# Optimization experiments

Hardware: AMD Instinct MI355X
Metric: run time of the kernel (lower is better)

The kernel has to match this reference:

```python
import jax, jax.numpy as jnp
import numpy as np

FRACTAL_OUTPUT = (5, 5)            # (a, b); requires 5 * num_kernels == a*b
PERC_THRESHOLD = 0.59275
NEXT_SHAPE = (224, 224)
K_END = int(0.4 * FRACTAL_OUTPUT[0] * FRACTAL_OUTPUT[1] + 1)   # 11
KERNEL_SIZES = list(range(3, K_END + 1, 2))                    # [3,5,7,9,11]


def setup_inputs() -> dict:
    key = jax.random.key(0)
    inputs = jax.random.uniform(key, (64, 224, 224, 3), dtype=jnp.float32) * 255.0
    return {"inputs": inputs}


def _extract_patches(x, k):
    # tf.image.extract_patches(sizes=strides=k, SAME) == zero-pad + space-to-depth
    B, H, W, C = x.shape
    rows, cols = -(-H // k), -(-W // k)
    ph, pw = rows * k - H, cols * k - W
    x = jnp.pad(x, ((0, 0), (ph // 2, ph - ph // 2), (pw // 2, pw - pw // 2), (0, 0)))
    x = x.reshape(B, rows, k, cols, k, C).transpose(0, 1, 3, 2, 4, 5)
    return x.reshape(B * rows * cols, k, k, C), rows * cols


def _binarize(patches, k, ch):
    # distance function: 1 iff |channel value - center pixel channel value| <= k
    center = patches[:, k // 2, k // 2, ch][:, None, None]
    return (jnp.abs(patches[..., ch] - center) <= k).astype(jnp.int32)


def _connected_stats(binp, k):
    # 4-connected components via min-label propagation (== tfa connected_components
    # up to relabeling; we only need #components and max label count incl. background)
    N = binp.shape[0]
    idx = jnp.arange(1, k * k + 1, dtype=jnp.int32).reshape(k, k)
    INF = jnp.int32(k * k + 2)
    lbl0 = jnp.where(binp > 0, idx, 0)

    def step(_, lbl):
        v = jnp.where(binp > 0, lbl, INF)
        pad = lambda a, w: jnp.pad(a, ((0, 0),) + w, constant_values=INF)
        up    = pad(v, ((1, 0), (0, 0)))[:, :-1, :]
        down  = pad(v, ((0, 1), (0, 0)))[:, 1:, :]
        left  = pad(v, ((0, 0), (1, 0)))[:, :, :-1]
        right = pad(v, ((0, 0), (0, 1)))[:, :, 1:]
        m = jnp.minimum(jnp.minimum(v, up), jnp.minimum(jnp.minimum(down, left), right))
        return jnp.where(binp > 0, m, 0)

    lbl = jax.lax.fori_loop(0, k * k, step, lbl0)  # k*k iters guarantee convergence
    ncomp = jnp.sum((binp > 0) & (lbl == idx), axis=(1, 2)).astype(jnp.int32)
    lblf = lbl.reshape(N, k * k)
    cnt = jnp.zeros((N, k * k + 1), jnp.int32).at[jnp.arange(N)[:, None], lblf].add(1)
    return ncomp, cnt.max(axis=1)  # (#components, most-common label count incl bg 0)


def _components(inputs, k, ch):
    B = inputs.shape[0]
    patches, P = _extract_patches(inputs, k)
    binp = _binarize(patches, k, ch)                    # (B*P, k, k)
    ones = binp.sum(axis=(1, 2)).reshape(B, P)          # int counts per patch
    # tf.bincount(minlength=1, maxlength=k*k): bins 0..k*k-1, value k*k dropped
    cnt = jnp.zeros((B, k * k + 1), jnp.float32).at[jnp.arange(B)[:, None], ones].add(1.0)
    prob = cnt[:, : k * k] / P                          # (B, k*k)
    n = jnp.arange(1, k * k + 1, dtype=jnp.float32)
    fd = (prob / n).sum(1)
    m = (prob * n).sum(1)
    m2 = ((prob * prob) * n).sum(1)
    lac = (m2 - m * m) / (m * m)
    perc = ((ones.astype(jnp.float32) / (k * k)) >= PERC_THRESHOLD).astype(jnp.int32)
    acp = perc.sum(1) // P                              # tf integer reduce_mean
    ncomp, marea = _connected_stats(binp, k)
    acn = ncomp.reshape(B, P).sum(1) // P
    acma = marea.reshape(B, P).sum(1) // P
    return jnp.stack([acn.astype(jnp.float32), acp.astype(jnp.float32),
                      acma.astype(jnp.float32), lac, fd], axis=1)   # (B, 5)


def _rearrange(c):
    # group metric-major: all acn over kernels, then acp, acma, lac, fd
    return jnp.concatenate([c[:, mm::5] for mm in range(5)], axis=1)


def reference(inputs):
    B = inputs.shape[0]
    chans = []
    for ch in range(3):
        comps = jnp.concatenate([_components(inputs, k, ch) for k in KERNEL_SIZES], axis=1)
        chans.append(_rearrange(comps).reshape(B, FRACTAL_OUTPUT[0], FRACTAL_OUTPUT[1]))
    out = jnp.stack(chans, axis=3)                      # (B, a, b, 3)
    return jax.image.resize(out, (B, NEXT_SHAPE[0], NEXT_SHAPE[1], 3), method='bilinear')
```

## Files before the change

kernel.cpp:

```cpp
#include <hip/hip_runtime.h>

#define HW 224
#define NIMG 64
#define NPIX ((size_t)NIMG * HW * HW)

typedef unsigned long long u64;

struct U128 { u64 lo, hi; };

__device__ __forceinline__ u64  u_or  (u64 a, u64 b){ return a | b; }
__device__ __forceinline__ u64  u_and (u64 a, u64 b){ return a & b; }
__device__ __forceinline__ u64  u_andn(u64 a, u64 b){ return a & ~b; }
__device__ __forceinline__ bool u_eq(u64 a, u64 b){ return a == b; }
__device__ __forceinline__ bool u_nz(u64 a){ return a != 0ull; }
__device__ __forceinline__ u64  u_shl(u64 a, int n){ return a << n; }
__device__ __forceinline__ u64  u_shr(u64 a, int n){ return a >> n; }
__device__ __forceinline__ int  u_pop(u64 a){ return __popcll(a); }
__device__ __forceinline__ u64  u_low(u64 a){ return a & (0ull - a); }

__device__ __forceinline__ U128 u_or  (U128 a, U128 b){ return {a.lo|b.lo, a.hi|b.hi}; }
__device__ __forceinline__ U128 u_and (U128 a, U128 b){ return {a.lo&b.lo, a.hi&b.hi}; }
__device__ __forceinline__ U128 u_andn(U128 a, U128 b){ return {a.lo&~b.lo, a.hi&~b.hi}; }
__device__ __forceinline__ bool u_eq(U128 a, U128 b){ return a.lo==b.lo && a.hi==b.hi; }
__device__ __forceinline__ bool u_nz(U128 a){ return (a.lo | a.hi) != 0ull; }
__device__ __forceinline__ U128 u_shl(U128 a, int n){
    return { a.lo << n, (a.hi << n) | (a.lo >> (64 - n)) };
}
__device__ __forceinline__ U128 u_shr(U128 a, int n){
    return { (a.lo >> n) | (a.hi << (64 - n)), a.hi >> n };
}
__device__ __forceinline__ int u_pop(U128 a){ return __popcll(a.lo) + __popcll(a.hi); }
__device__ __forceinline__ U128 u_low(U128 a){
    if (a.lo) return { a.lo & (0ull - a.lo), 0ull };
    return { 0ull, a.hi & (0ull - a.hi) };
}

template<bool B, class T, class F> struct sel        { using type = T; };
template<class T, class F>         struct sel<false, T, F> { using type = F; };

template<int K>
__device__ __forceinline__ void load_row(const float* __restrict__ p, float* r) {
#pragma unroll
    for (int j = 0; j + 4 <= K; j += 4) {
        float4 v; __builtin_memcpy(&v, p + j, 16);
        r[j] = v.x; r[j + 1] = v.y; r[j + 2] = v.z; r[j + 3] = v.w;
    }
    if constexpr ((K & 3) >= 2) {
        constexpr int b = (K / 4) * 4;
        float2 v; __builtin_memcpy(&v, p + b, 8);
        r[b] = v.x; r[b + 1] = v.y;
    }
    if constexpr (K & 1) r[K - 1] = p[K - 1];
}

template<int K, int S>
__device__ __forceinline__ void stats_body(const float* __restrict__ img,
                                           float* __restrict__ o,
                                           int hist[4][124], int* sums) {
    constexpr int KK   = K * K;
    constexpr int ROWS = (HW + K - 1) / K;
    constexpr int P    = ROWS * ROWS;
    constexpr int PAD  = (ROWS * K - HW) / 2;
    using M = typename sel<(KK <= 64), u64, U128>::type;
    const int wid = threadIdx.x >> 6;

    u64 lcl = 0, lch = 0, rcl = 0, rch = 0;
#pragma unroll
    for (int i = 0; i < K; i++) {
        const int cl = i * K, cr = i * K + K - 1;
        if (cl < 64) lcl |= 1ull << cl; else lch |= 1ull << (cl - 64);
        if (cr < 64) rcl |= 1ull << cr; else rch |= 1ull << (cr - 64);
    }
    M leftCol, rightCol;
    if constexpr (KK <= 64) { leftCol = lcl; rightCol = rcl; }
    else { leftCol = U128{lcl, lch}; rightCol = U128{rcl, rch}; }

    int t_perc = 0, t_ncomp = 0, t_marea = 0;

    for (int p = threadIdx.x; p < P; p += 256) {
        const int pr = p / ROWS, pc = p - pr * ROWS;
        const int y0 = pr * K - PAD, x0 = pc * K - PAD;
        const float cen = img[((size_t)(y0 + K / 2) * HW + (x0 + K / 2)) * S];

        M msk;
        if constexpr (KK <= 64) msk = 0ull; else msk = U128{0, 0};

        const bool fast = (S == 1) && (y0 >= 0) && (x0 >= 0) &&
                          (y0 + K <= HW) && (x0 + K <= HW);
        if (fast) {
#pragma unroll
            for (int i = 0; i < K; i++) {
                float r[K];
                load_row<K>(img + (size_t)(y0 + i) * HW + x0, r);
#pragma unroll
                for (int j = 0; j < K; j++) {
                    const u64 bit = (fabsf(r[j] - cen) <= (float)K) ? 1ull : 0ull;
                    const int cb = i * K + j;
                    if constexpr (KK <= 64) msk |= bit << cb;
                    else { if (cb < 64) msk.lo |= bit << cb; else msk.hi |= bit << (cb - 64); }
                }
            }
        } else {
#pragma unroll
            for (int i = 0; i < K; i++) {
                const int y = y0 + i;
                const bool yin = (unsigned)y < (unsigned)HW;
#pragma unroll
                for (int j = 0; j < K; j++) {
                    const int x = x0 + j;
                    const bool inb = yin && ((unsigned)x < (unsigned)HW);
                    const float v = inb ? img[((size_t)y * HW + x) * S] : 0.0f;
                    const u64 bit = (fabsf(v - cen) <= (float)K) ? 1ull : 0ull;
                    const int cb = i * K + j;
                    if constexpr (KK <= 64) msk |= bit << cb;
                    else { if (cb < 64) msk.lo |= bit << cb; else msk.hi |= bit << (cb - 64); }
                }
            }
        }
        const int ones = u_pop(msk);

        M nbm = u_or(u_or(u_shl(u_andn(msk, rightCol), 1),
                          u_shr(u_andn(msk, leftCol ), 1)),
                     u_or(u_shl(msk, K), u_shr(msk, K)));
        M iso = u_andn(msk, nbm);
        const int niso = u_pop(iso);
        int ncomp = niso, maxsz = (niso > 0) ? 1 : 0;
        M m = u_andn(msk, iso);
        while (u_nz(m)) {
            M s = u_low(m);
            for (;;) {
                M g = u_or(s, u_or(u_or(u_shl(u_andn(s, rightCol), 1),
                                        u_shr(u_andn(s, leftCol ), 1)),
                                   u_or(u_shl(s, K), u_shr(s, K))));
                g = u_and(g, m);
                if (u_eq(g, s)) break;
                s = g;
            }
            ncomp++;
            const int sz = u_pop(s);
            if (sz > maxsz) maxsz = sz;
            m = u_andn(m, s);
        }

        const int bgcnt = KK - ones;
        const int marea = (bgcnt > maxsz) ? bgcnt : maxsz;

        t_ncomp += ncomp;
        t_marea += marea;
        if ((float)ones / (float)KK >= 0.59275f) t_perc++;
        atomicAdd(&hist[wid][ones], 1);
    }

    atomicAdd(&sums[0], t_perc);
    atomicAdd(&sums[1], t_ncomp);
    atomicAdd(&sums[2], t_marea);
    __syncthreads();

    if (threadIdx.x == 0) {
        const float Pf = (float)P;
        float fd = 0.0f, m1 = 0.0f, m2 = 0.0f;
        for (int s = 0; s < KK; s++) {
            const float prob = (float)(hist[0][s] + hist[1][s] + hist[2][s] + hist[3][s]) / Pf;
            const float n = (float)(s + 1);
            fd += prob / n;
            m1 += prob * n;
            m2 += prob * prob * n;
        }
        const float lac = (m2 - m1 * m1) / (m1 * m1);
        o[0]  = (float)(sums[1] / P);
        o[15] = (float)(sums[0] / P);
        o[30] = (float)(sums[2] / P);
        o[45] = lac;
        o[60] = fd;
    }
}

template<int S>
__global__ __launch_bounds__(256) void fractal_stats(const float* __restrict__ in,
                                                     float* __restrict__ interm) {
    const int b    = blockIdx.x / 15;
    const int rem  = blockIdx.x % 15;
    const int ch   = rem / 5;
    const int kidx = rem % 5;

    __shared__ int hist[4][124];
    __shared__ int sums[3];
    for (int i = threadIdx.x; i < 4 * 124; i += 256) ((int*)hist)[i] = 0;
    if (threadIdx.x < 3) sums[threadIdx.x] = 0;
    __syncthreads();

    const float* img = (S == 1) ? in + ((size_t)ch * NIMG + b) * HW * HW
                                : in + (size_t)b * HW * HW * 3 + ch;
    float* o = interm + (size_t)b * 75 + kidx * 3 + ch;

    switch (kidx) {
        case 0: stats_body<3,  S>(img, o, hist, sums); break;
        case 1: stats_body<5,  S>(img, o, hist, sums); break;
        case 2: stats_body<7,  S>(img, o, hist, sums); break;
        case 3: stats_body<9,  S>(img, o, hist, sums); break;
        case 4: stats_body<11, S>(img, o, hist, sums); break;
    }
}

__global__ __launch_bounds__(256) void deinterleave(const float* __restrict__ in,
                                                    float* __restrict__ planes) {
    const size_t pix = ((size_t)blockIdx.x * 256 + threadIdx.x) * 4;
    if (pix >= NPIX) return;
    float4 a, b, c;
    __builtin_memcpy(&a, in + pix * 3,     16);
    __builtin_memcpy(&b, in + pix * 3 + 4, 16);
    __builtin_memcpy(&c, in + pix * 3 + 8, 16);
    const float4 p0 = make_float4(a.x, a.w, b.z, c.y);
    const float4 p1 = make_float4(a.y, b.x, b.w, c.z);
    const float4 p2 = make_float4(a.z, b.y, c.x, c.w);
    __builtin_memcpy(planes + pix,            &p0, 16);
    __builtin_memcpy(planes + NPIX + pix,     &p1, 16);
    __builtin_memcpy(planes + 2 * NPIX + pix, &p2, 16);
}

__global__ __launch_bounds__(256) void fractal_resize(const float* __restrict__ interm,
                                                      float* __restrict__ out, int total) {
    const int idx = blockIdx.x * 256 + threadIdx.x;
    if (idx >= total) return;
    const int ch = idx % 3;
    int t = idx / 3;
    const int x = t % HW; t /= HW;
    const int y = t % HW;
    const int b = t / HW;

    const float sc = 5.0f / 224.0f;
    const float uy = ((float)y + 0.5f) * sc - 0.5f;
    const float ux = ((float)x + 0.5f) * sc - 0.5f;

    const float fy = floorf(uy), fx = floorf(ux);
    const float wy = uy - fy,    wx = ux - fx;
    int y0 = (int)fy, x0 = (int)fx;
    int y1 = y0 + 1,  x1 = x0 + 1;
    if (y0 < 0) y0 = 0; if (x0 < 0) x0 = 0;
    if (y1 > 4) y1 = 4; if (x1 > 4) x1 = 4;

    const float* g = interm + (size_t)b * 75 + ch;
    const float v00 = g[(y0 * 5 + x0) * 3];
    const float v01 = g[(y0 * 5 + x1) * 3];
    const float v10 = g[(y1 * 5 + x0) * 3];
    const float v11 = g[(y1 * 5 + x1) * 3];

    out[idx] = (1.0f - wy) * ((1.0f - wx) * v00 + wx * v01)
             +         wy  * ((1.0f - wx) * v10 + wx * v11);
}

extern "C" void kernel_launch(void* const* d_in, const int* in_sizes, int n_in,
                              void* d_out, int out_size, void* d_ws, size_t ws_size,
                              hipStream_t stream) {
    const float* in = (const float*)d_in[0];
    float* out = (float*)d_out;
    float* interm = (float*)d_ws;

    const size_t planes_off = 19456;
    const size_t need = planes_off + 3 * NPIX * sizeof(float);

    if (ws_size >= need) {
        float* planes = (float*)((char*)d_ws + planes_off);
        deinterleave<<<(int)(NPIX / 4 / 256), 256, 0, stream>>>(in, planes);
        fractal_stats<1><<<NIMG * 15, 256, 0, stream>>>(planes, interm);
    } else {
        fractal_stats<3><<<NIMG * 15, 256, 0, stream>>>(in, interm);
    }
    fractal_resize<<<(out_size + 255) / 256, 256, 0, stream>>>(interm, out, out_size);
}
```

Baseline: 177.6 us.

## Split patch work into 8 slices per combo with 64-thread blocks and global accumulation

The stats kernel now launches 7680 single-wavefront blocks instead of 960 256-thread blocks. Each block handles one eighth of the patches of one (image, channel, kernel) combination and merges its histogram and sums into a global int accumulator with atomics. A new finalize kernel then computes the lacunarity, fractal dimension and averages from that accumulator. The aim is better load balance and occupancy across CUs, because small-K combos previously had uneven per-block work. In exchange it adds one extra kernel launch, global atomics, and accumulator zeroing folded into the deinterleave kernel.

```diff
diff --git a/kernel.cpp b/kernel.cpp
--- a/kernel.cpp
+++ b/kernel.cpp
@@ -3,6 +3,10 @@
 #define HW 224
 #define NIMG 64
 #define NPIX ((size_t)NIMG * HW * HW)
+#define NSLICE 8
+#define ACC_STRIDE 128
+#define NCOMBO (NIMG * 15)
+#define ACC_BYTES (NCOMBO * ACC_STRIDE * 4)
 
 typedef unsigned long long u64;
 
@@ -53,103 +57,223 @@
     if constexpr (K & 1) r[K - 1] = p[K - 1];
 }
 
-template<int K, int S>
-__device__ __forceinline__ void stats_body(const float* __restrict__ img,
-                                           float* __restrict__ o,
-                                           int hist[4][124], int* sums) {
+template<int K, int S, class M>
+__device__ __forceinline__ void do_patch(const float* __restrict__ img, int p,
+                                         M leftCol, M rightCol,
+                                         int* hist, int& t_perc, int& t_ncomp,
+                                         int& t_marea) {
     constexpr int KK   = K * K;
     constexpr int ROWS = (HW + K - 1) / K;
-    constexpr int P    = ROWS * ROWS;
     constexpr int PAD  = (ROWS * K - HW) / 2;
-    using M = typename sel<(KK <= 64), u64, U128>::type;
-    const int wid = threadIdx.x >> 6;
-
-    u64 lcl = 0, lch = 0, rcl = 0, rch = 0;
+
+    const int pr = p / ROWS, pc = p - pr * ROWS;
+    const int y0 = pr * K - PAD, x0 = pc * K - PAD;
+    const float cen = img[((size_t)(y0 + K / 2) * HW + (x0 + K / 2)) * S];
+
+    M msk;
+    if constexpr (KK <= 64) msk = 0ull; else msk = U128{0, 0};
+
+    const bool fast = (S == 1) && (y0 >= 0) && (x0 >= 0) &&
+                      (y0 + K <= HW) && (x0 + K <= HW);
+    if (fast) {
+#pragma unroll
+        for (int i = 0; i < K; i++) {
+            float r[K];
+            load_row<K>(img + (size_t)(y0 + i) * HW + x0, r);
+#pragma unroll
+            for (int j = 0; j < K; j++) {
+                const u64 bit = (fabsf(r[j] - cen) <= (float)K) ? 1ull : 0ull;
+                const int cb = i * K + j;
+                if constexpr (KK <= 64) msk |= bit << cb;
+                else { if (cb < 64) msk.lo |= bit << cb; else msk.hi |= bit << (cb - 64); }
+            }
+        }
+    } else {
+#pragma unroll
+        for (int i = 0; i < K; i++) {
+            const int y = y0 + i;
+            const bool yin = (unsigned)y < (unsigned)HW;
+#pragma unroll
+            for (int j = 0; j < K; j++) {
+                const int x = x0 + j;
+                const bool inb = yin && ((unsigned)x < (unsigned)HW);
+                const float v = inb ? img[((size_t)y * HW + x) * S] : 0.0f;
+                const u64 bit = (fabsf(v - cen) <= (float)K) ? 1ull : 0ull;
+                const int cb = i * K + j;
+                if constexpr (KK <= 64) msk |= bit << cb;
+                else { if (cb < 64) msk.lo |= bit << cb; else msk.hi |= bit << (cb - 64); }
+            }
+        }
+    }
+    const int ones = u_pop(msk);
+
+    M nbm = u_or(u_or(u_shl(u_andn(msk, rightCol), 1),
+                      u_shr(u_andn(msk, leftCol ), 1)),
+                 u_or(u_shl(msk, K), u_shr(msk, K)));
+    M iso = u_andn(msk, nbm);
+    const int niso = u_pop(iso);
+    int ncomp = niso, maxsz = (niso > 0) ? 1 : 0;
+    M m = u_andn(msk, iso);
+    while (u_nz(m)) {
+        M s = u_low(m);
+        for (;;) {
+            M g = u_or(s, u_or(u_or(u_shl(u_andn(s, rightCol), 1),
+                                    u_shr(u_andn(s, leftCol ), 1)),
+                               u_or(u_shl(s, K), u_shr(s, K))));
+            g = u_and(g, m);
+            if (u_eq(g, s)) break;
+            s = g;
+        }
+        ncomp++;
+        const int sz = u_pop(s);
+        if (sz > maxsz) maxsz = sz;
+        m = u_andn(m, s);
+    }
+
+    const int bgcnt = KK - ones;
+    const int marea = (bgcnt > maxsz) ? bgcnt : maxsz;
+    t_ncomp += ncomp;
+    t_marea += marea;
+    if ((float)ones / (float)KK >= 0.59275f) t_perc++;
+    atomicAdd(&hist[ones], 1);
+}
+
+template<int K>
+__device__ __forceinline__ void make_colmasks(u64& lcl, u64& lch, u64& rcl, u64& rch) {
+    lcl = lch = rcl = rch = 0;
 #pragma unroll
     for (int i = 0; i < K; i++) {
         const int cl = i * K, cr = i * K + K - 1;
         if (cl < 64) lcl |= 1ull << cl; else lch |= 1ull << (cl - 64);
         if (cr < 64) rcl |= 1ull << cr; else rch |= 1ull << (cr - 64);
     }
+}
+
+template<int K, int S>
+__device__ __forceinline__ void stats_body(const float* __restrict__ img,
+                                           int slice, int* hist,
+                                           int* __restrict__ gout) {
+    constexpr int KK   = K * K;
+    constexpr int ROWS = (HW + K - 1) / K;
+    constexpr int P    = ROWS * ROWS;
+    using M = typename sel<(KK <= 64), u64, U128>::type;
+
+    u64 lcl, lch, rcl, rch;
+    make_colmasks<K>(lcl, lch, rcl, rch);
     M leftCol, rightCol;
     if constexpr (KK <= 64) { leftCol = lcl; rightCol = rcl; }
     else { leftCol = U128{lcl, lch}; rightCol = U128{rcl, rch}; }
 
+    for (int s = threadIdx.x; s <= KK; s += 64) hist[s] = 0;
+    __syncthreads();
+
+    const int pstart = (slice * P) / NSLICE;
+    const int pend   = ((slice + 1) * P) / NSLICE;
+
     int t_perc = 0, t_ncomp = 0, t_marea = 0;
-
-    for (int p = threadIdx.x; p < P; p += 256) {
-        const int pr = p / ROWS, pc = p - pr * ROWS;
-        const int y0 = pr * K - PAD, x0 = pc * K - PAD;
-        const float cen = img[((size_t)(y0 + K / 2) * HW + (x0 + K / 2)) * S];
-
-        M msk;
-        if constexpr (KK <= 64) msk = 0ull; else msk = U128{0, 0};
-
-        const bool fast = (S == 1) && (y0 >= 0) && (x0 >= 0) &&
-                          (y0 + K <= HW) && (x0 + K <= HW);
-        if (fast) {
-#pragma unroll
-            for (int i = 0; i < K; i++) {
-                float r[K];
-                load_row<K>(img + (size_t)(y0 + i) * HW + x0, r);
-#pragma unroll
-                for (int j = 0; j < K; j++) {
-                    const u64 bit = (fabsf(r[j] - cen) <= (float)K) ? 1ull : 0ull;
-                    const int cb = i * K + j;
-                    if constexpr (KK <= 64) msk |= bit << cb;
-                    else { if (cb < 64) msk.lo |= bit << cb; else msk.hi |= bit << (cb - 64); }
-                }
-            }
-        } else {
-#pragma unroll
-            for (int i = 0; i < K; i++) {
-                const int y = y0 + i;
-                const bool yin = (unsigned)y < (unsigned)HW;
-#pragma unroll
-                for (int j = 0; j < K; j++) {
-                    const int x = x0 + j;
-                    const bool inb = yin && ((unsigned)x < (unsigned)HW);
-                    const float v = inb ? img[((size_t)y * HW + x) * S] : 0.0f;
-                    const u64 bit = (fabsf(v - cen) <= (float)K) ? 1ull : 0ull;
-                    const int cb = i * K + j;
-                    if constexpr (KK <= 64) msk |= bit << cb;
-                    else { if (cb < 64) msk.lo |= bit << cb; else msk.hi |= bit << (cb - 64); }
-                }
-            }
-        }
-        const int ones = u_pop(msk);
-
-        M nbm = u_or(u_or(u_shl(u_andn(msk, rightCol), 1),
-                          u_shr(u_andn(msk, leftCol ), 1)),
-                     u_or(u_shl(msk, K), u_shr(msk, K)));
-        M iso = u_andn(msk, nbm);
-        const int niso = u_pop(iso);
-        int ncomp = niso, maxsz = (niso > 0) ? 1 : 0;
-        M m = u_andn(msk, iso);
-        while (u_nz(m)) {
-            M s = u_low(m);
-            for (;;) {
-                M g = u_or(s, u_or(u_or(u_shl(u_andn(s, rightCol), 1),
-                                        u_shr(u_andn(s, leftCol ), 1)),
-                                   u_or(u_shl(s, K), u_shr(s, K))));
-                g = u_and(g, m);
-                if (u_eq(g, s)) break;
-                s = g;
-            }
-            ncomp++;
-            const int sz = u_pop(s);
-            if (sz > maxsz) maxsz = sz;
-            m = u_andn(m, s);
-        }
-
-        const int bgcnt = KK - ones;
-        const int marea = (bgcnt > maxsz) ? bgcnt : maxsz;
-
-        t_ncomp += ncomp;
-        t_marea += marea;
-        if ((float)ones / (float)KK >= 0.59275f) t_perc++;
-        atomicAdd(&hist[wid][ones], 1);
-    }
+    for (int p = pstart + threadIdx.x; p < pend; p += 64)
+        do_patch<K, S, M>(img, p, leftCol, rightCol, hist, t_perc, t_ncomp, t_marea);
+
+#pragma unroll
+    for (int off = 32; off; off >>= 1) {
+        t_perc  += __shfl_down(t_perc,  off);
+        t_ncomp += __shfl_down(t_ncomp, off);
+        t_marea += __shfl_down(t_marea, off);
+    }
+    __syncthreads();
+
+    for (int s = threadIdx.x; s <= KK; s += 64) {
+        const int v = hist[s];
+        if (v) atomicAdd(&gout[s], v);
+    }
+    if (threadIdx.x == 0) {
+        atomicAdd(&gout[124], t_perc);
+        atomicAdd(&gout[125], t_ncomp);
+        atomicAdd(&gout[126], t_marea);
+    }
+}
+
+template<int S>
+__global__ __launch_bounds__(64) void fractal_stats(const float* __restrict__ in,
+                                                    int* __restrict__ gacc) {
+    const int B     = blockIdx.x;
+    const int x     = B & 7;
+    const int j     = B >> 3;
+    const int gl    = j / 40;
+    const int inner = j - gl * 40;
+    const int g     = gl * 8 + x;
+    const int b     = g / 3, ch = g - b * 3;
+    const int kidx  = inner >> 3;
+    const int slice = inner & 7;
+
+    __shared__ int hist[124];
+
+    const float* img = (S == 1) ? in + ((size_t)ch * NIMG + b) * HW * HW
+                                : in + (size_t)b * HW * HW * 3 + ch;
+    int* gout = gacc + (g * 5 + kidx) * ACC_STRIDE;
+
+    switch (kidx) {
+        case 0: stats_body<3,  S>(img, slice, hist, gout); break;
+        case 1: stats_body<5,  S>(img, slice, hist, gout); break;
+        case 2: stats_body<7,  S>(img, slice, hist, gout); break;
+        case 3: stats_body<9,  S>(img, slice, hist, gout); break;
+        case 4: stats_body<11, S>(img, slice, hist, gout); break;
+    }
+}
+
+__global__ __launch_bounds__(64) void fractal_finalize(const int* __restrict__ gacc,
+                                                       float* __restrict__ interm) {
+    const int cidx = blockIdx.x * 64 + threadIdx.x;
+    if (cidx >= NCOMBO) return;
+    const int b    = cidx / 15;
+    const int rem  = cidx % 15;
+    const int ch   = rem / 5;
+    const int kidx = rem % 5;
+    const int K    = 3 + 2 * kidx;
+    const int ROWS = (HW + K - 1) / K;
+    const int P    = ROWS * ROWS;
+    const int KK   = K * K;
+
+    const int* a = gacc + cidx * ACC_STRIDE;
+    const float Pf = (float)P;
+    float fd = 0.0f, m1 = 0.0f, m2 = 0.0f;
+    for (int s = 0; s < KK; s++) {
+        const float prob = (float)a[s] / Pf;
+        const float n = (float)(s + 1);
+        fd += prob / n;
+        m1 += prob * n;
+        m2 += prob * prob * n;
+    }
+    const float lac = (m2 - m1 * m1) / (m1 * m1);
+
+    float* o = interm + (size_t)b * 75 + kidx * 3 + ch;
+    o[0]  = (float)(a[125] / P);
+    o[15] = (float)(a[124] / P);
+    o[30] = (float)(a[126] / P);
+    o[45] = lac;
+    o[60] = fd;
+}
+
+template<int K, int S>
+__device__ __forceinline__ void stats_body_full(const float* __restrict__ img,
+                                                float* __restrict__ o,
+                                                int hist4[4][124], int* sums) {
+    constexpr int KK   = K * K;
+    constexpr int ROWS = (HW + K - 1) / K;
+    constexpr int P    = ROWS * ROWS;
+    using M = typename sel<(KK <= 64), u64, U128>::type;
+    const int wid = threadIdx.x >> 6;
+
+    u64 lcl, lch, rcl, rch;
+    make_colmasks<K>(lcl, lch, rcl, rch);
+    M leftCol, rightCol;
+    if constexpr (KK <= 64) { leftCol = lcl; rightCol = rcl; }
+    else { leftCol = U128{lcl, lch}; rightCol = U128{rcl, rch}; }
+
+    int t_perc = 0, t_ncomp = 0, t_marea = 0;
+    for (int p = threadIdx.x; p < P; p += 256)
+        do_patch<K, S, M>(img, p, leftCol, rightCol, hist4[wid],
+                          t_perc, t_ncomp, t_marea);
 
     atomicAdd(&sums[0], t_perc);
     atomicAdd(&sums[1], t_ncomp);
@@ -160,7 +284,7 @@
         const float Pf = (float)P;
         float fd = 0.0f, m1 = 0.0f, m2 = 0.0f;
         for (int s = 0; s < KK; s++) {
-            const float prob = (float)(hist[0][s] + hist[1][s] + hist[2][s] + hist[3][s]) / Pf;
+            const float prob = (float)(hist4[0][s] + hist4[1][s] + hist4[2][s] + hist4[3][s]) / Pf;
             const float n = (float)(s + 1);
             fd += prob / n;
             m1 += prob * n;
@@ -176,8 +300,8 @@
 }
 
 template<int S>
-__global__ __launch_bounds__(256) void fractal_stats(const float* __restrict__ in,
-                                                     float* __restrict__ interm) {
+__global__ __launch_bounds__(256) void fractal_stats_full(const float* __restrict__ in,
+                                                          float* __restrict__ interm) {
     const int b    = blockIdx.x / 15;
     const int rem  = blockIdx.x % 15;
     const int ch   = rem / 5;
@@ -189,22 +313,27 @@
     if (threadIdx.x < 3) sums[threadIdx.x] = 0;
     __syncthreads();
 
-    const float* img = (S == 1) ? in + ((size_t)ch * NIMG + b) * HW * HW
-                                : in + (size_t)b * HW * HW * 3 + ch;
+    const float* img = in + (size_t)b * HW * HW * 3 + ch;
     float* o = interm + (size_t)b * 75 + kidx * 3 + ch;
 
     switch (kidx) {
-        case 0: stats_body<3,  S>(img, o, hist, sums); break;
-        case 1: stats_body<5,  S>(img, o, hist, sums); break;
-        case 2: stats_body<7,  S>(img, o, hist, sums); break;
-        case 3: stats_body<9,  S>(img, o, hist, sums); break;
-        case 4: stats_body<11, S>(img, o, hist, sums); break;
+        case 0: stats_body_full<3,  S>(img, o, hist, sums); break;
+        case 1: stats_body_full<5,  S>(img, o, hist, sums); break;
+        case 2: stats_body_full<7,  S>(img, o, hist, sums); break;
+        case 3: stats_body_full<9,  S>(img, o, hist, sums); break;
+        case 4: stats_body_full<11, S>(img, o, hist, sums); break;
     }
 }
 
 __global__ __launch_bounds__(256) void deinterleave(const float* __restrict__ in,
-                                                    float* __restrict__ planes) {
-    const size_t pix = ((size_t)blockIdx.x * 256 + threadIdx.x) * 4;
+                                                    float* __restrict__ planes,
+                                                    int* __restrict__ gacc) {
+    const int t = blockIdx.x * 256 + threadIdx.x;
+    if (t < ACC_BYTES / 16) {
+        const int4 z = make_int4(0, 0, 0, 0);
+        ((int4*)gacc)[t] = z;
+    }
+    const size_t pix = (size_t)t * 4;
     if (pix >= NPIX) return;
     float4 a, b, c;
     __builtin_memcpy(&a, in + pix * 3,     16);
@@ -256,15 +385,18 @@
     float* out = (float*)d_out;
     float* interm = (float*)d_ws;
 
-    const size_t planes_off = 19456;
+    const size_t acc_off    = 19456;
+    const size_t planes_off = acc_off + ACC_BYTES;
     const size_t need = planes_off + 3 * NPIX * sizeof(float);
 
     if (ws_size >= need) {
+        int*   gacc   = (int*)((char*)d_ws + acc_off);
         float* planes = (float*)((char*)d_ws + planes_off);
-        deinterleave<<<(int)(NPIX / 4 / 256), 256, 0, stream>>>(in, planes);
-        fractal_stats<1><<<NIMG * 15, 256, 0, stream>>>(planes, interm);
+        deinterleave<<<(int)(NPIX / 4 / 256), 256, 0, stream>>>(in, planes, gacc);
+        fractal_stats<1><<<192 * 40, 64, 0, stream>>>(planes, gacc);
+        fractal_finalize<<<(NCOMBO + 63) / 64, 64, 0, stream>>>(gacc, interm);
     } else {
-        fractal_stats<3><<<NIMG * 15, 256, 0, stream>>>(in, interm);
+        fractal_stats_full<3><<<NIMG * 15, 256, 0, stream>>>(in, interm);
     }
     fractal_resize<<<(out_size + 255) / 256, 256, 0, stream>>>(interm, out, out_size);
 }
```

Measured after the change: 164.5 us. 7.4% less time.
